# Performance work log

Measured on AMD Instinct MI355X. Metric: run time of the kernel, lower is better.

Reference implementation:

```python
import jax, jax.numpy as jnp
import numpy as np

EPS = 1e-8


def setup_inputs() -> dict:
    B, L, K = 512, 4096, 4
    key = jax.random.key(0)
    k1, k2, k3, k4 = jax.random.split(key, 4)
    # observations: Bernoulli-like values in [0,1] (math is valid for soft obs too)
    obs = (jax.random.uniform(k1, (B, L), dtype=jnp.float32) > 0.5).astype(jnp.float32)
    mask = jnp.ones((B, L), dtype=bool)
    # normalized HMM parameters, as _normalize_params produces
    start = jax.random.uniform(k2, (K,), dtype=jnp.float32) + EPS
    start = start / start.sum()
    trans = jax.random.uniform(k3, (K, K), dtype=jnp.float32) + EPS
    trans = trans / trans.sum(axis=1, keepdims=True)
    emission = jnp.clip(jax.random.uniform(k4, (K,), dtype=jnp.float32), EPS, 1.0 - EPS)
    return {"obs": obs, "mask": mask, "start": start, "trans": trans, "emission": emission}


def _forward_backward(obs, mask, start, trans, emission):
    B, L = obs.shape
    K = start.shape[0]
    # log Bernoulli emission: (B, L, K); masked (missing) positions contribute 0
    logp = jnp.log(emission + EPS)
    log1mp = jnp.log1p(-emission + EPS)
    logB = obs[:, :, None] * logp + (1.0 - obs[:, :, None]) * log1mp
    logB = jnp.where(mask[:, :, None], logB, 0.0)

    logA = jnp.log(trans + EPS)            # (K, K)
    logstart = jnp.log(start + EPS)        # (K,)

    logB_t = jnp.transpose(logB, (1, 0, 2))  # (L, B, K)

    # forward recurrence: alpha_t[j] = logsumexp_i(alpha_{t-1}[i] + logA[i,j]) + logB_t[j]
    alpha0 = logstart[None, :] + logB_t[0]  # (B, K)

    def fstep(alpha_prev, logb_t):
        a = jax.nn.logsumexp(alpha_prev[:, :, None] + logA[None, :, :], axis=1) + logb_t
        return a, a

    _, alphas = jax.lax.scan(fstep, alpha0, logB_t[1:])
    alpha = jnp.concatenate([alpha0[None], alphas], axis=0)  # (L, B, K)

    # backward recurrence: beta_t[i] = logsumexp_j(logA[i,j] + logB_{t+1}[j] + beta_{t+1}[j])
    betaL = jnp.zeros((B, K), dtype=obs.dtype)

    def bstep(beta_next, logb_next):
        b = jax.nn.logsumexp(logA[None, :, :] + (logb_next + beta_next)[:, None, :], axis=2)
        return b, b

    _, betas = jax.lax.scan(bstep, betaL, logB_t[1:], reverse=True)
    beta = jnp.concatenate([betas, betaL[None]], axis=0)  # (L, B, K)

    alpha = jnp.transpose(alpha, (1, 0, 2))  # (B, L, K)
    beta = jnp.transpose(beta, (1, 0, 2))    # (B, L, K)

    # per-sequence log-likelihood at last valid timestep
    lengths = mask.sum(axis=1).astype(jnp.int32)
    last_idx = jnp.clip(lengths - 1, 0, L - 1)
    final_alpha = alpha[jnp.arange(B), last_idx]  # (B, K)
    seq_loglikes = jax.nn.logsumexp(final_alpha, axis=1)

    # posterior marginals gamma = softmax(alpha + beta) over states
    gamma = jax.nn.softmax(alpha + beta, axis=-1)
    return gamma, seq_loglikes


def reference(obs, mask, start, trans, emission):
    return _forward_backward(obs, mask, start, trans, emission)
```

## Files before the change

kernel.cpp:

```cpp
#include <hip/hip_runtime.h>


#define BB 512
#define LL 4096
#define NT 512
#define SS 8
#define NW 8
#define EPSF 1e-8f
#define LN2F 0.6931471805599453f
#define HST 20

static_assert(NT * SS == LL, "chunking");

typedef float f4raw __attribute__((ext_vector_type(4)));

__device__ __forceinline__ float rcp_(float x) { return __builtin_amdgcn_rcpf(x); }
__device__ __forceinline__ float log_(float x) { return LN2F * __builtin_amdgcn_logf(x); }

__device__ __forceinline__ void mm16(const float* X, const float* Y, float* Z) {
#pragma unroll
    for (int i = 0; i < 4; i++)
#pragma unroll
        for (int j = 0; j < 4; j++)
            Z[i * 4 + j] = (X[i * 4 + 0] * Y[0 + j] + X[i * 4 + 1] * Y[4 + j]) +
                           (X[i * 4 + 2] * Y[8 + j] + X[i * 4 + 3] * Y[12 + j]);
}
__device__ __forceinline__ void nrm16(float* Z) {
    float s = 0.f;
#pragma unroll
    for (int k = 0; k < 16; k++) s += Z[k];
    float r = rcp_(s);
#pragma unroll
    for (int k = 0; k < 16; k++) Z[k] *= r;
}

__global__ __launch_bounds__(NT, 4) void k_fb(const float* __restrict__ obs,
                                              const float* __restrict__ start_,
                                              const float* __restrict__ trans,
                                              const float* __restrict__ emission,
                                              float* __restrict__ gamma,
                                              float* __restrict__ ll) {
    const int b = blockIdx.x;
    const int c = threadIdx.x;
    const int lane = c & 63;
    const int wv = c >> 6;

    __shared__ f4raw gbuf[NT * SS];
    __shared__ float H4[16][HST];
    __shared__ float H4f[16][HST];
    __shared__ float totF[NW][16];
    __shared__ float totB[NW][16];
    __shared__ float bndA[NW][4];
    __shared__ float bndB[NW][4];
    __shared__ float llred[NW];

    float A[16], pe[4], qe[4], sv[4];
#pragma unroll
    for (int k = 0; k < 16; k++) A[k] = trans[k] + EPSF;
#pragma unroll
    for (int j = 0; j < 4; j++) {
        float e = emission[j];
        pe[j] = e + EPSF;
        qe[j] = 1.0f - e + EPSF;
    }
    {
        float s = 0.f;
#pragma unroll
        for (int j = 0; j < 4; j++) { sv[j] = start_[j] + EPSF; s += sv[j]; }
        float r = rcp_(s);
#pragma unroll
        for (int j = 0; j < 4; j++) sv[j] *= r;
    }

    const float4* op = (const float4*)(obs + (size_t)b * LL + c * SS);
    float4 oa = op[0], ob2 = op[1];
    unsigned bits = (oa.x > 0.5f ? 1u : 0u) | (oa.y > 0.5f ? 2u : 0u) |
                    (oa.z > 0.5f ? 4u : 0u) | (oa.w > 0.5f ? 8u : 0u) |
                    (ob2.x > 0.5f ? 16u : 0u) | (ob2.y > 0.5f ? 32u : 0u) |
                    (ob2.z > 0.5f ? 64u : 0u) | (ob2.w > 0.5f ? 128u : 0u);

    if (c < 32) {
        const int o = c & 15;
        const bool first = c >= 16;
        float Mt[16];
        {
            float b0[4];
            int o0 = o & 1;
#pragma unroll
            for (int j = 0; j < 4; j++) b0[j] = o0 ? pe[j] : qe[j];
            if (first) {
#pragma unroll
                for (int k = 0; k < 16; k++) Mt[k] = 0.f;
#pragma unroll
                for (int j = 0; j < 4; j++) Mt[j * 4 + j] = b0[j];
            } else {
#pragma unroll
                for (int i = 0; i < 4; i++)
#pragma unroll
                    for (int j = 0; j < 4; j++) Mt[i * 4 + j] = A[i * 4 + j] * b0[j];
            }
        }
#pragma unroll
        for (int u = 1; u < 4; u++) {
            int ou = (o >> u) & 1;
            float bu[4];
#pragma unroll
            for (int j = 0; j < 4; j++) bu[j] = ou ? pe[j] : qe[j];
            float Zt[16];
#pragma unroll
            for (int i = 0; i < 4; i++)
#pragma unroll
                for (int j = 0; j < 4; j++)
                    Zt[i * 4 + j] = ((Mt[i * 4 + 0] * A[0 + j] + Mt[i * 4 + 1] * A[4 + j]) +
                                     (Mt[i * 4 + 2] * A[8 + j] + Mt[i * 4 + 3] * A[12 + j])) * bu[j];
#pragma unroll
            for (int k = 0; k < 16; k++) Mt[k] = Zt[k];
        }
        nrm16(Mt);
        float* dst = first ? &H4f[o][0] : &H4[o][0];
#pragma unroll
        for (int k = 0; k < 16; k++) dst[k] = Mt[k];
    }
    __syncthreads();

    float P[16];
    {
        const int i1 = bits & 15, i2 = (bits >> 4) & 15;
        const float* Xp = (c == 0) ? &H4f[i1][0] : &H4[i1][0];
        float X[16], Y[16];
#pragma unroll
        for (int k = 0; k < 16; k++) { X[k] = Xp[k]; Y[k] = H4[i2][k]; }
        mm16(X, Y, P);
        nrm16(P);
    }

    float M[16];
#pragma unroll
    for (int k = 0; k < 16; k++) M[k] = P[k];
#pragma unroll
    for (int d = 1; d < 64; d <<= 1) {
        int src = lane - d;
        int s2 = src < 0 ? 0 : src;
        float Up[16];
#pragma unroll
        for (int r = 0; r < 16; r++) Up[r] = __shfl(M[r], s2, 64);
        float Z[16];
        mm16(Up, M, Z);
        bool ok = lane >= d;
#pragma unroll
        for (int k = 0; k < 16; k++) M[k] = ok ? Z[k] : M[k];
        if (d == 2 || d == 8 || d == 32) nrm16(M);
    }
    if (lane == 63) {
#pragma unroll
        for (int r = 0; r < 16; r++) totF[wv][r] = M[r];
    }
    __syncthreads();
    if (wv > 0) {
        float E[16];
#pragma unroll
        for (int k = 0; k < 16; k++) E[k] = totF[0][k];
        for (int w = 1; w < wv; w++) {
            float Z[16];
            mm16(E, &totF[w][0], Z);
#pragma unroll
            for (int k = 0; k < 16; k++) E[k] = Z[k];
        }
        float Z[16];
        mm16(E, M, Z);
#pragma unroll
        for (int k = 0; k < 16; k++) M[k] = Z[k];
    }
    nrm16(M);
    float vprev[4];
    {
        float vn[4];
#pragma unroll
        for (int j = 0; j < 4; j++)
            vn[j] = (sv[0] * M[0 + j] + sv[1] * M[4 + j]) +
                    (sv[2] * M[8 + j] + sv[3] * M[12 + j]);
        float r = rcp_((vn[0] + vn[1]) + (vn[2] + vn[3]));
#pragma unroll
        for (int j = 0; j < 4; j++) vn[j] *= r;
#pragma unroll
        for (int j = 0; j < 4; j++) vprev[j] = __shfl_up(vn[j], 1, 64);
        if (lane == 63) {
#pragma unroll
            for (int j = 0; j < 4; j++) bndA[wv][j] = vn[j];
        }
    }

#pragma unroll
    for (int k = 0; k < 16; k++) M[k] = P[k];
#pragma unroll
    for (int d = 1; d < 64; d <<= 1) {
        int src = lane + d;
        int s2 = src > 63 ? 63 : src;
        float Rt[16];
#pragma unroll
        for (int r = 0; r < 16; r++) Rt[r] = __shfl(M[r], s2, 64);
        float Z[16];
        mm16(M, Rt, Z);
        bool ok = (lane + d) <= 63;
#pragma unroll
        for (int k = 0; k < 16; k++) M[k] = ok ? Z[k] : M[k];
        if (d == 2 || d == 8 || d == 32) nrm16(M);
    }
    if (lane == 0) {
#pragma unroll
        for (int r = 0; r < 16; r++) totB[wv][r] = M[r];
    }
    __syncthreads();
    if (wv < NW - 1) {
        float S[16];
#pragma unroll
        for (int k = 0; k < 16; k++) S[k] = totB[wv + 1][k];
        for (int w = wv + 2; w < NW; w++) {
            float Z[16];
            mm16(S, &totB[w][0], Z);
#pragma unroll
            for (int k = 0; k < 16; k++) S[k] = Z[k];
        }
        float Z[16];
        mm16(M, S, Z);
#pragma unroll
        for (int k = 0; k < 16; k++) M[k] = Z[k];
    }
    nrm16(M);
    float bnext[4];
    {
        float un[4];
#pragma unroll
        for (int i = 0; i < 4; i++)
            un[i] = (M[i * 4 + 0] + M[i * 4 + 1]) + (M[i * 4 + 2] + M[i * 4 + 3]);
        float r = rcp_((un[0] + un[1]) + (un[2] + un[3]));
#pragma unroll
        for (int i = 0; i < 4; i++) un[i] *= r;
#pragma unroll
        for (int i = 0; i < 4; i++) bnext[i] = __shfl_down(un[i], 1, 64);
        if (lane == 0) {
#pragma unroll
            for (int i = 0; i < 4; i++) bndB[wv][i] = un[i];
        }
    }
    __syncthreads();

    float av[4];
#pragma unroll
    for (int j = 0; j < 4; j++) av[j] = vprev[j];
    if (lane == 0 && wv > 0) {
#pragma unroll
        for (int j = 0; j < 4; j++) av[j] = bndA[wv - 1][j];
    }
    if (c == 0) {
#pragma unroll
        for (int j = 0; j < 4; j++) av[j] = sv[j];
    }
    float be[4];
#pragma unroll
    for (int i = 0; i < 4; i++) be[i] = bnext[i];
    if (lane == 63 && wv < NW - 1) {
#pragma unroll
        for (int i = 0; i < 4; i++) be[i] = bndB[wv + 1][i];
    }
    if (c == NT - 1) {
#pragma unroll
        for (int i = 0; i < 4; i++) be[i] = 1.0f;
    }

    const int lrow = wv * 512 + lane * SS;
    float llp = 0.f;
#pragma unroll
    for (int s = 0; s < SS; s++) {
        float bb[4];
#pragma unroll
        for (int j = 0; j < 4; j++) bb[j] = ((bits >> s) & 1u) ? pe[j] : qe[j];
        float w[4];
        if (s == 0 && c == 0) {
#pragma unroll
            for (int j = 0; j < 4; j++) w[j] = av[j] * bb[j];
        } else {
#pragma unroll
            for (int j = 0; j < 4; j++)
                w[j] = ((av[0] * A[0 + j] + av[1] * A[4 + j]) +
                        (av[2] * A[8 + j] + av[3] * A[12 + j])) * bb[j];
        }
#pragma unroll
        for (int j = 0; j < 4; j++) av[j] = w[j];
        f4raw st; st.x = av[0]; st.y = av[1]; st.z = av[2]; st.w = av[3];
        gbuf[lrow + (s ^ (lane & 7))] = st;
        if (s == 3 || s == SS - 1) {
            float sm = (av[0] + av[1]) + (av[2] + av[3]);
            llp += log_(sm);
            float r = rcp_(sm);
#pragma unroll
            for (int j = 0; j < 4; j++) av[j] *= r;
        }
    }

#pragma unroll
    for (int s = SS - 1; s >= 0; s--) {
        const int idx = lrow + (s ^ (lane & 7));
        f4raw avv = gbuf[idx];
        float g0 = avv.x * be[0], g1 = avv.y * be[1];
        float g2 = avv.z * be[2], g3 = avv.w * be[3];
        float rg = rcp_((g0 + g1) + (g2 + g3));
        f4raw gv; gv.x = g0 * rg; gv.y = g1 * rg; gv.z = g2 * rg; gv.w = g3 * rg;
        gbuf[idx] = gv;

        float bb[4];
#pragma unroll
        for (int j = 0; j < 4; j++) bb[j] = ((bits >> s) & 1u) ? pe[j] : qe[j];
        float e0 = bb[0] * be[0], e1 = bb[1] * be[1];
        float e2 = bb[2] * be[2], e3 = bb[3] * be[3];
#pragma unroll
        for (int i = 0; i < 4; i++)
            be[i] = (A[i * 4 + 0] * e0 + A[i * 4 + 1] * e1) +
                    (A[i * 4 + 2] * e2 + A[i * 4 + 3] * e3);
        if (s == 4 || s == 0) {
            float r = rcp_((be[0] + be[1]) + (be[2] + be[3]));
#pragma unroll
            for (int i = 0; i < 4; i++) be[i] *= r;
        }
    }

    {
        f4raw* gout = (f4raw*)gamma + (size_t)b * 4096 + wv * 512;
#pragma unroll
        for (int k = 0; k < SS; k++) {
            int i = k * 64 + lane;
            int owner = i >> 3;
            int sw = (i & 7) ^ (owner & 7);
            f4raw v = gbuf[wv * 512 + owner * 8 + sw];
            __builtin_nontemporal_store(v, gout + i);
        }
    }

#pragma unroll
    for (int off = 32; off > 0; off >>= 1) llp += __shfl_down(llp, off, 64);
    if (lane == 0) llred[wv] = llp;
    __syncthreads();
    if (c == 0) {
        float t = 0.f;
#pragma unroll
        for (int w = 0; w < NW; w++) t += llred[w];
        ll[b] = t;
    }
}

extern "C" void kernel_launch(void* const* d_in, const int* in_sizes, int n_in,
                              void* d_out, int out_size, void* d_ws, size_t ws_size,
                              hipStream_t stream) {
    const float* obs      = (const float*)d_in[0];
    const float* start    = (const float*)d_in[2];
    const float* trans    = (const float*)d_in[3];
    const float* emission = (const float*)d_in[4];

    float* out   = (float*)d_out;
    float* gamma = out;
    float* ll    = out + (size_t)BB * LL * 4;

    k_fb<<<dim3(BB), dim3(NT), 0, stream>>>(obs, start, trans, emission, gamma, ll);
}
```

Baseline: 98.14 us.

## Split fused forward-backward kernel into scan and replay kernels via workspace

Splits the single kernel into two. A scan kernel computes per-chunk forward and backward boundary vectors and writes them to workspace memory. It also computes the log-likelihood from tracked log-scale factors rather than a per-step reduction. A replay kernel then runs with 256-thread blocks and twice as many blocks, recomputes the local recurrences and writes gamma. This is meant to shrink the LDS footprint and register pressure so more blocks fit per CU, at the cost of a second launch, re-reading obs and a workspace round trip.

```diff
diff --git a/kernel.cpp b/kernel.cpp
--- a/kernel.cpp
+++ b/kernel.cpp
@@ -3,14 +3,15 @@
 
 #define BB 512
 #define LL 4096
-#define NT 512
+#define NT1 512
 #define SS 8
-#define NW 8
+#define NW1 8
+#define NT2 256
 #define EPSF 1e-8f
 #define LN2F 0.6931471805599453f
 #define HST 20
 
-static_assert(NT * SS == LL, "chunking");
+static_assert(NT1 * SS == LL, "chunking");
 
 typedef float f4raw __attribute__((ext_vector_type(4)));
 
@@ -25,44 +26,37 @@
             Z[i * 4 + j] = (X[i * 4 + 0] * Y[0 + j] + X[i * 4 + 1] * Y[4 + j]) +
                            (X[i * 4 + 2] * Y[8 + j] + X[i * 4 + 3] * Y[12 + j]);
 }
-__device__ __forceinline__ void nrm16(float* Z) {
+__device__ __forceinline__ float nrm16s(float* Z) {
     float s = 0.f;
 #pragma unroll
     for (int k = 0; k < 16; k++) s += Z[k];
     float r = rcp_(s);
 #pragma unroll
     for (int k = 0; k < 16; k++) Z[k] *= r;
-}
-
-__global__ __launch_bounds__(NT, 4) void k_fb(const float* __restrict__ obs,
-                                              const float* __restrict__ start_,
-                                              const float* __restrict__ trans,
-                                              const float* __restrict__ emission,
-                                              float* __restrict__ gamma,
-                                              float* __restrict__ ll) {
+    return s;
+}
+
+__global__ __launch_bounds__(NT1, 4) void k_scan(const float* __restrict__ obs,
+                                                 const float* __restrict__ start_,
+                                                 const float* __restrict__ trans,
+                                                 const float* __restrict__ emission,
+                                                 f4raw* __restrict__ a_in,
+                                                 f4raw* __restrict__ b_in,
+                                                 float* __restrict__ ll) {
     const int b = blockIdx.x;
     const int c = threadIdx.x;
     const int lane = c & 63;
     const int wv = c >> 6;
 
-    __shared__ f4raw gbuf[NT * SS];
     __shared__ float H4[16][HST];
     __shared__ float H4f[16][HST];
-    __shared__ float totF[NW][16];
-    __shared__ float totB[NW][16];
-    __shared__ float bndA[NW][4];
-    __shared__ float bndB[NW][4];
-    __shared__ float llred[NW];
-
-    float A[16], pe[4], qe[4], sv[4];
-#pragma unroll
-    for (int k = 0; k < 16; k++) A[k] = trans[k] + EPSF;
-#pragma unroll
-    for (int j = 0; j < 4; j++) {
-        float e = emission[j];
-        pe[j] = e + EPSF;
-        qe[j] = 1.0f - e + EPSF;
-    }
+    __shared__ float totF[NW1][17];
+    __shared__ float totB[NW1][16];
+
+    const float4* op = (const float4*)(obs + (size_t)b * LL + c * SS);
+    float4 oa = op[0], ob2 = op[1];
+
+    float sv[4];
     {
         float s = 0.f;
 #pragma unroll
@@ -72,14 +66,21 @@
         for (int j = 0; j < 4; j++) sv[j] *= r;
     }
 
-    const float4* op = (const float4*)(obs + (size_t)b * LL + c * SS);
-    float4 oa = op[0], ob2 = op[1];
     unsigned bits = (oa.x > 0.5f ? 1u : 0u) | (oa.y > 0.5f ? 2u : 0u) |
                     (oa.z > 0.5f ? 4u : 0u) | (oa.w > 0.5f ? 8u : 0u) |
                     (ob2.x > 0.5f ? 16u : 0u) | (ob2.y > 0.5f ? 32u : 0u) |
                     (ob2.z > 0.5f ? 64u : 0u) | (ob2.w > 0.5f ? 128u : 0u);
 
     if (c < 32) {
+        float A[16], pe[4], qe[4];
+#pragma unroll
+        for (int k = 0; k < 16; k++) A[k] = trans[k] + EPSF;
+#pragma unroll
+        for (int j = 0; j < 4; j++) {
+            float e = emission[j];
+            pe[j] = e + EPSF;
+            qe[j] = 1.0f - e + EPSF;
+        }
         const int o = c & 15;
         const bool first = c >= 16;
         float Mt[16];
@@ -116,25 +117,25 @@
 #pragma unroll
             for (int k = 0; k < 16; k++) Mt[k] = Zt[k];
         }
-        nrm16(Mt);
+        float s = nrm16s(Mt);
         float* dst = first ? &H4f[o][0] : &H4[o][0];
 #pragma unroll
         for (int k = 0; k < 16; k++) dst[k] = Mt[k];
+        dst[16] = log_(s);
     }
     __syncthreads();
 
     float P[16];
+    float Lp;
     {
         const int i1 = bits & 15, i2 = (bits >> 4) & 15;
         const float* Xp = (c == 0) ? &H4f[i1][0] : &H4[i1][0];
-        float X[16], Y[16];
-#pragma unroll
-        for (int k = 0; k < 16; k++) { X[k] = Xp[k]; Y[k] = H4[i2][k]; }
-        mm16(X, Y, P);
-        nrm16(P);
-    }
-
-    float M[16];
+        const float* Yp = &H4[i2][0];
+        mm16(Xp, Yp, P);
+        Lp = Xp[16] + Yp[16] + log_(nrm16s(P));
+    }
+
+    float M[16], Lm = Lp;
 #pragma unroll
     for (int k = 0; k < 16; k++) M[k] = P[k];
 #pragma unroll
@@ -144,25 +145,30 @@
         float Up[16];
 #pragma unroll
         for (int r = 0; r < 16; r++) Up[r] = __shfl(M[r], s2, 64);
+        float Lup = __shfl(Lm, s2, 64);
         float Z[16];
         mm16(Up, M, Z);
         bool ok = lane >= d;
 #pragma unroll
         for (int k = 0; k < 16; k++) M[k] = ok ? Z[k] : M[k];
-        if (d == 2 || d == 8 || d == 32) nrm16(M);
+        Lm = ok ? (Lup + Lm) : Lm;
+        if (d == 2 || d == 8 || d == 32) Lm += log_(nrm16s(M));
     }
     if (lane == 63) {
 #pragma unroll
         for (int r = 0; r < 16; r++) totF[wv][r] = M[r];
+        totF[wv][16] = Lm;
     }
     __syncthreads();
     if (wv > 0) {
         float E[16];
+        float LE = totF[0][16];
 #pragma unroll
         for (int k = 0; k < 16; k++) E[k] = totF[0][k];
         for (int w = 1; w < wv; w++) {
             float Z[16];
             mm16(E, &totF[w][0], Z);
+            LE += totF[w][16];
 #pragma unroll
             for (int k = 0; k < 16; k++) E[k] = Z[k];
         }
@@ -170,23 +176,28 @@
         mm16(E, M, Z);
 #pragma unroll
         for (int k = 0; k < 16; k++) M[k] = Z[k];
-    }
-    nrm16(M);
-    float vprev[4];
+        Lm += LE;
+    }
+    Lm += log_(nrm16s(M));
+
     {
         float vn[4];
 #pragma unroll
         for (int j = 0; j < 4; j++)
             vn[j] = (sv[0] * M[0 + j] + sv[1] * M[4 + j]) +
                     (sv[2] * M[8 + j] + sv[3] * M[12 + j]);
-        float r = rcp_((vn[0] + vn[1]) + (vn[2] + vn[3]));
-#pragma unroll
-        for (int j = 0; j < 4; j++) vn[j] *= r;
-#pragma unroll
-        for (int j = 0; j < 4; j++) vprev[j] = __shfl_up(vn[j], 1, 64);
-        if (lane == 63) {
-#pragma unroll
-            for (int j = 0; j < 4; j++) bndA[wv][j] = vn[j];
+        float s = (vn[0] + vn[1]) + (vn[2] + vn[3]);
+        f4raw* arow = a_in + (size_t)b * NT1;
+        if (c == NT1 - 1) {
+            ll[b] = log_(s) + Lm;
+        } else {
+            float r = rcp_(s);
+            f4raw v; v.x = vn[0] * r; v.y = vn[1] * r; v.z = vn[2] * r; v.w = vn[3] * r;
+            arow[c + 1] = v;
+        }
+        if (c == 0) {
+            f4raw v; v.x = sv[0]; v.y = sv[1]; v.z = sv[2]; v.w = sv[3];
+            arow[0] = v;
         }
     }
 
@@ -204,18 +215,18 @@
         bool ok = (lane + d) <= 63;
 #pragma unroll
         for (int k = 0; k < 16; k++) M[k] = ok ? Z[k] : M[k];
-        if (d == 2 || d == 8 || d == 32) nrm16(M);
+        if (d == 2 || d == 8 || d == 32) nrm16s(M);
     }
     if (lane == 0) {
 #pragma unroll
         for (int r = 0; r < 16; r++) totB[wv][r] = M[r];
     }
     __syncthreads();
-    if (wv < NW - 1) {
+    if (wv < NW1 - 1) {
         float S[16];
 #pragma unroll
         for (int k = 0; k < 16; k++) S[k] = totB[wv + 1][k];
-        for (int w = wv + 2; w < NW; w++) {
+        for (int w = wv + 2; w < NW1; w++) {
             float Z[16];
             mm16(S, &totB[w][0], Z);
 #pragma unroll
@@ -226,50 +237,63 @@
 #pragma unroll
         for (int k = 0; k < 16; k++) M[k] = Z[k];
     }
-    nrm16(M);
-    float bnext[4];
+    nrm16s(M);
     {
         float un[4];
 #pragma unroll
         for (int i = 0; i < 4; i++)
             un[i] = (M[i * 4 + 0] + M[i * 4 + 1]) + (M[i * 4 + 2] + M[i * 4 + 3]);
         float r = rcp_((un[0] + un[1]) + (un[2] + un[3]));
-#pragma unroll
-        for (int i = 0; i < 4; i++) un[i] *= r;
-#pragma unroll
-        for (int i = 0; i < 4; i++) bnext[i] = __shfl_down(un[i], 1, 64);
-        if (lane == 0) {
-#pragma unroll
-            for (int i = 0; i < 4; i++) bndB[wv][i] = un[i];
-        }
-    }
-    __syncthreads();
-
-    float av[4];
-#pragma unroll
-    for (int j = 0; j < 4; j++) av[j] = vprev[j];
-    if (lane == 0 && wv > 0) {
-#pragma unroll
-        for (int j = 0; j < 4; j++) av[j] = bndA[wv - 1][j];
-    }
-    if (c == 0) {
-#pragma unroll
-        for (int j = 0; j < 4; j++) av[j] = sv[j];
-    }
-    float be[4];
-#pragma unroll
-    for (int i = 0; i < 4; i++) be[i] = bnext[i];
-    if (lane == 63 && wv < NW - 1) {
-#pragma unroll
-        for (int i = 0; i < 4; i++) be[i] = bndB[wv + 1][i];
-    }
-    if (c == NT - 1) {
-#pragma unroll
-        for (int i = 0; i < 4; i++) be[i] = 1.0f;
-    }
+        f4raw* brow = b_in + (size_t)b * NT1;
+        if (c > 0) {
+            f4raw v; v.x = un[0] * r; v.y = un[1] * r; v.z = un[2] * r; v.w = un[3] * r;
+            brow[c - 1] = v;
+        }
+        if (c == NT1 - 1) {
+            f4raw v; v.x = 1.f; v.y = 1.f; v.z = 1.f; v.w = 1.f;
+            brow[NT1 - 1] = v;
+        }
+    }
+}
+
+__global__ __launch_bounds__(NT2, 4) void k_replay(const float* __restrict__ obs,
+                                                   const float* __restrict__ trans,
+                                                   const float* __restrict__ emission,
+                                                   const f4raw* __restrict__ a_in,
+                                                   const f4raw* __restrict__ b_in,
+                                                   float* __restrict__ gamma) {
+    const int bid = blockIdx.x;
+    const int b = bid >> 1;
+    const int h = bid & 1;
+    const int t = threadIdx.x;
+    const int lane = t & 63;
+    const int wv = t >> 6;
+    const int c = h * NT2 + t;
+
+    __shared__ f4raw gbuf[NT2 * SS];
+
+    float A[16], pe[4], qe[4];
+#pragma unroll
+    for (int k = 0; k < 16; k++) A[k] = trans[k] + EPSF;
+#pragma unroll
+    for (int j = 0; j < 4; j++) {
+        float e = emission[j];
+        pe[j] = e + EPSF;
+        qe[j] = 1.0f - e + EPSF;
+    }
+
+    const float4* op = (const float4*)(obs + (size_t)b * LL + (size_t)c * SS);
+    float4 oa = op[0], ob2 = op[1];
+    unsigned bits = (oa.x > 0.5f ? 1u : 0u) | (oa.y > 0.5f ? 2u : 0u) |
+                    (oa.z > 0.5f ? 4u : 0u) | (oa.w > 0.5f ? 8u : 0u) |
+                    (ob2.x > 0.5f ? 16u : 0u) | (ob2.y > 0.5f ? 32u : 0u) |
+                    (ob2.z > 0.5f ? 64u : 0u) | (ob2.w > 0.5f ? 128u : 0u);
+
+    f4raw av4 = a_in[(size_t)b * NT1 + c];
+    f4raw be4 = b_in[(size_t)b * NT1 + c];
+    float av[4] = {av4.x, av4.y, av4.z, av4.w};
 
     const int lrow = wv * 512 + lane * SS;
-    float llp = 0.f;
 #pragma unroll
     for (int s = 0; s < SS; s++) {
         float bb[4];
@@ -289,15 +313,14 @@
         for (int j = 0; j < 4; j++) av[j] = w[j];
         f4raw st; st.x = av[0]; st.y = av[1]; st.z = av[2]; st.w = av[3];
         gbuf[lrow + (s ^ (lane & 7))] = st;
-        if (s == 3 || s == SS - 1) {
-            float sm = (av[0] + av[1]) + (av[2] + av[3]);
-            llp += log_(sm);
-            float r = rcp_(sm);
+        if ((s & 3) == 3) {
+            float r = rcp_((av[0] + av[1]) + (av[2] + av[3]));
 #pragma unroll
             for (int j = 0; j < 4; j++) av[j] *= r;
         }
     }
 
+    float be[4] = {be4.x, be4.y, be4.z, be4.w};
 #pragma unroll
     for (int s = SS - 1; s >= 0; s--) {
         const int idx = lrow + (s ^ (lane & 7));
@@ -317,7 +340,7 @@
         for (int i = 0; i < 4; i++)
             be[i] = (A[i * 4 + 0] * e0 + A[i * 4 + 1] * e1) +
                     (A[i * 4 + 2] * e2 + A[i * 4 + 3] * e3);
-        if (s == 4 || s == 0) {
+        if ((s & 3) == 0) {
             float r = rcp_((be[0] + be[1]) + (be[2] + be[3]));
 #pragma unroll
             for (int i = 0; i < 4; i++) be[i] *= r;
@@ -325,7 +348,7 @@
     }
 
     {
-        f4raw* gout = (f4raw*)gamma + (size_t)b * 4096 + wv * 512;
+        f4raw* gout = (f4raw*)gamma + (size_t)b * 4096 + h * 2048 + wv * 512;
 #pragma unroll
         for (int k = 0; k < SS; k++) {
             int i = k * 64 + lane;
@@ -334,17 +357,6 @@
             f4raw v = gbuf[wv * 512 + owner * 8 + sw];
             __builtin_nontemporal_store(v, gout + i);
         }
-    }
-
-#pragma unroll
-    for (int off = 32; off > 0; off >>= 1) llp += __shfl_down(llp, off, 64);
-    if (lane == 0) llred[wv] = llp;
-    __syncthreads();
-    if (c == 0) {
-        float t = 0.f;
-#pragma unroll
-        for (int w = 0; w < NW; w++) t += llred[w];
-        ll[b] = t;
     }
 }
 
@@ -360,5 +372,9 @@
     float* gamma = out;
     float* ll    = out + (size_t)BB * LL * 4;
 
-    k_fb<<<dim3(BB), dim3(NT), 0, stream>>>(obs, start, trans, emission, gamma, ll);
-}
+    f4raw* a_in = (f4raw*)d_ws;
+    f4raw* b_in = a_in + (size_t)BB * NT1;
+
+    k_scan<<<dim3(BB), dim3(NT1), 0, stream>>>(obs, start, trans, emission, a_in, b_in, ll);
+    k_replay<<<dim3(2 * BB), dim3(NT2), 0, stream>>>(obs, trans, emission, a_in, b_in, gamma);
+}
```

After: 107.3 us. 9.4% more time.

## Build chunk matrices directly per thread and fuse forward/backward wave scans

Applied to the files above, without the earlier changes.

Each thread now computes its 8-step transfer matrix directly instead of going through a shared table of 4-step lookup matrices, which removes one block barrier and the shared-memory lookup. The forward and backward 64-lane shuffle scans are interleaved in a single loop, and the two separate barrier phases are merged into one. The log-likelihood is carried as an accumulated log-scale through the scan, so the final shuffle and shared reduction plus their barrier go away. The cost is more per-thread FLOPs for the matrix build and higher register pressure from holding both scan matrices at once.

```diff
diff --git a/kernel.cpp b/kernel.cpp
--- a/kernel.cpp
+++ b/kernel.cpp
@@ -8,7 +8,6 @@
 #define NW 8
 #define EPSF 1e-8f
 #define LN2F 0.6931471805599453f
-#define HST 20
 
 static_assert(NT * SS == LL, "chunking");
 
@@ -25,13 +24,14 @@
             Z[i * 4 + j] = (X[i * 4 + 0] * Y[0 + j] + X[i * 4 + 1] * Y[4 + j]) +
                            (X[i * 4 + 2] * Y[8 + j] + X[i * 4 + 3] * Y[12 + j]);
 }
-__device__ __forceinline__ void nrm16(float* Z) {
+__device__ __forceinline__ float nrm16s(float* Z) {
     float s = 0.f;
 #pragma unroll
     for (int k = 0; k < 16; k++) s += Z[k];
     float r = rcp_(s);
 #pragma unroll
     for (int k = 0; k < 16; k++) Z[k] *= r;
+    return s;
 }
 
 __global__ __launch_bounds__(NT, 4) void k_fb(const float* __restrict__ obs,
@@ -46,15 +46,203 @@
     const int wv = c >> 6;
 
     __shared__ f4raw gbuf[NT * SS];
-    __shared__ float H4[16][HST];
-    __shared__ float H4f[16][HST];
-    __shared__ float totF[NW][16];
+    __shared__ float totF[NW][17];
     __shared__ float totB[NW][16];
-    __shared__ float bndA[NW][4];
-    __shared__ float bndB[NW][4];
-    __shared__ float llred[NW];
-
-    float A[16], pe[4], qe[4], sv[4];
+
+    const float4* op = (const float4*)(obs + (size_t)b * LL + c * SS);
+    float4 oa = op[0], ob2 = op[1];
+
+    float sv[4];
+    {
+        float s = 0.f;
+#pragma unroll
+        for (int j = 0; j < 4; j++) { sv[j] = start_[j] + EPSF; s += sv[j]; }
+        float r = rcp_(s);
+#pragma unroll
+        for (int j = 0; j < 4; j++) sv[j] *= r;
+    }
+
+    unsigned bits = (oa.x > 0.5f ? 1u : 0u) | (oa.y > 0.5f ? 2u : 0u) |
+                    (oa.z > 0.5f ? 4u : 0u) | (oa.w > 0.5f ? 8u : 0u) |
+                    (ob2.x > 0.5f ? 16u : 0u) | (ob2.y > 0.5f ? 32u : 0u) |
+                    (ob2.z > 0.5f ? 64u : 0u) | (ob2.w > 0.5f ? 128u : 0u);
+
+    float P[16];
+    float Lp = 0.f;
+    {
+        float A[16], pe[4], qe[4];
+#pragma unroll
+        for (int k = 0; k < 16; k++) A[k] = trans[k] + EPSF;
+#pragma unroll
+        for (int j = 0; j < 4; j++) {
+            float e = emission[j];
+            pe[j] = e + EPSF;
+            qe[j] = 1.0f - e + EPSF;
+        }
+        {
+            float bb[4];
+#pragma unroll
+            for (int j = 0; j < 4; j++) bb[j] = (bits & 1u) ? pe[j] : qe[j];
+            if (c == 0) {
+#pragma unroll
+                for (int i = 0; i < 4; i++)
+#pragma unroll
+                    for (int j = 0; j < 4; j++) P[i * 4 + j] = (i == j) ? bb[j] : 0.f;
+            } else {
+#pragma unroll
+                for (int i = 0; i < 4; i++)
+#pragma unroll
+                    for (int j = 0; j < 4; j++) P[i * 4 + j] = A[i * 4 + j] * bb[j];
+            }
+        }
+#pragma unroll
+        for (int s = 1; s < SS; s++) {
+            float bb[4];
+#pragma unroll
+            for (int j = 0; j < 4; j++) bb[j] = ((bits >> s) & 1u) ? pe[j] : qe[j];
+            float T[16];
+#pragma unroll
+            for (int i = 0; i < 4; i++)
+#pragma unroll
+                for (int j = 0; j < 4; j++)
+                    T[i * 4 + j] = ((P[i * 4 + 0] * A[0 + j] + P[i * 4 + 1] * A[4 + j]) +
+                                    (P[i * 4 + 2] * A[8 + j] + P[i * 4 + 3] * A[12 + j])) * bb[j];
+#pragma unroll
+            for (int k = 0; k < 16; k++) P[k] = T[k];
+            if (s == 3 || s == SS - 1) Lp += log_(nrm16s(P));
+        }
+    }
+
+    float Mf[16], Mb[16], Lm = Lp;
+#pragma unroll
+    for (int k = 0; k < 16; k++) { Mf[k] = P[k]; Mb[k] = P[k]; }
+#pragma unroll
+    for (int d = 1; d < 64; d <<= 1) {
+        const int sF = (lane >= d) ? (lane - d) : 0;
+        const int sB = (lane + d <= 63) ? (lane + d) : 63;
+        float UF[16], UB[16];
+#pragma unroll
+        for (int r = 0; r < 16; r++) UF[r] = __shfl(Mf[r], sF, 64);
+        float LF = __shfl(Lm, sF, 64);
+#pragma unroll
+        for (int r = 0; r < 16; r++) UB[r] = __shfl(Mb[r], sB, 64);
+        float Z[16];
+        mm16(UF, Mf, Z);
+        const bool okF = (lane >= d);
+#pragma unroll
+        for (int k = 0; k < 16; k++) Mf[k] = okF ? Z[k] : Mf[k];
+        Lm = okF ? (LF + Lm) : Lm;
+        mm16(Mb, UB, Z);
+        const bool okB = (lane + d <= 63);
+#pragma unroll
+        for (int k = 0; k < 16; k++) Mb[k] = okB ? Z[k] : Mb[k];
+        if (d == 2 || d == 8 || d == 32) { Lm += log_(nrm16s(Mf)); nrm16s(Mb); }
+    }
+    if (lane == 63) {
+#pragma unroll
+        for (int r = 0; r < 16; r++) totF[wv][r] = Mf[r];
+        totF[wv][16] = Lm;
+    }
+    if (lane == 0) {
+#pragma unroll
+        for (int r = 0; r < 16; r++) totB[wv][r] = Mb[r];
+    }
+    __syncthreads();
+
+    float vprev[4];
+    {
+        float E[16];
+        if (wv > 0) {
+            float LE = totF[0][16];
+#pragma unroll
+            for (int k = 0; k < 16; k++) E[k] = totF[0][k];
+            for (int w = 1; w < wv; w++) {
+                float Z[16];
+                mm16(E, &totF[w][0], Z);
+                LE += totF[w][16];
+#pragma unroll
+                for (int k = 0; k < 16; k++) E[k] = Z[k];
+            }
+            float Z[16];
+            mm16(E, Mf, Z);
+#pragma unroll
+            for (int k = 0; k < 16; k++) Mf[k] = Z[k];
+            Lm += LE;
+        }
+        Lm += log_(nrm16s(Mf));
+        float vn[4];
+#pragma unroll
+        for (int j = 0; j < 4; j++)
+            vn[j] = (sv[0] * Mf[0 + j] + sv[1] * Mf[4 + j]) +
+                    (sv[2] * Mf[8 + j] + sv[3] * Mf[12 + j]);
+        float s = (vn[0] + vn[1]) + (vn[2] + vn[3]);
+        if (c == NT - 1) ll[b] = log_(s) + Lm;
+        float r = rcp_(s);
+#pragma unroll
+        for (int j = 0; j < 4; j++) vn[j] *= r;
+#pragma unroll
+        for (int j = 0; j < 4; j++) vprev[j] = __shfl_up(vn[j], 1, 64);
+        if (lane == 0) {
+            if (wv == 0) {
+#pragma unroll
+                for (int j = 0; j < 4; j++) vprev[j] = sv[j];
+            } else {
+                float vp[4];
+#pragma unroll
+                for (int j = 0; j < 4; j++)
+                    vp[j] = (sv[0] * E[0 + j] + sv[1] * E[4 + j]) +
+                            (sv[2] * E[8 + j] + sv[3] * E[12 + j]);
+                float rr = rcp_((vp[0] + vp[1]) + (vp[2] + vp[3]));
+#pragma unroll
+                for (int j = 0; j < 4; j++) vprev[j] = vp[j] * rr;
+            }
+        }
+    }
+
+    float bnext[4];
+    {
+        float S[16];
+        if (wv < NW - 1) {
+#pragma unroll
+            for (int k = 0; k < 16; k++) S[k] = totB[wv + 1][k];
+            for (int w = wv + 2; w < NW; w++) {
+                float Z[16];
+                mm16(S, &totB[w][0], Z);
+#pragma unroll
+                for (int k = 0; k < 16; k++) S[k] = Z[k];
+            }
+            float Z[16];
+            mm16(Mb, S, Z);
+#pragma unroll
+            for (int k = 0; k < 16; k++) Mb[k] = Z[k];
+        }
+        nrm16s(Mb);
+        float u[4];
+#pragma unroll
+        for (int i = 0; i < 4; i++)
+            u[i] = (Mb[i * 4 + 0] + Mb[i * 4 + 1]) + (Mb[i * 4 + 2] + Mb[i * 4 + 3]);
+        float r = rcp_((u[0] + u[1]) + (u[2] + u[3]));
+#pragma unroll
+        for (int i = 0; i < 4; i++) u[i] *= r;
+#pragma unroll
+        for (int i = 0; i < 4; i++) bnext[i] = __shfl_down(u[i], 1, 64);
+        if (lane == 63) {
+            if (wv == NW - 1) {
+#pragma unroll
+                for (int i = 0; i < 4; i++) bnext[i] = 0.25f;
+            } else {
+                float bn[4];
+#pragma unroll
+                for (int i = 0; i < 4; i++)
+                    bn[i] = (S[i * 4 + 0] + S[i * 4 + 1]) + (S[i * 4 + 2] + S[i * 4 + 3]);
+                float rr = rcp_((bn[0] + bn[1]) + (bn[2] + bn[3]));
+#pragma unroll
+                for (int i = 0; i < 4; i++) bnext[i] = bn[i] * rr;
+            }
+        }
+    }
+
+    float A[16], pe[4], qe[4];
 #pragma unroll
     for (int k = 0; k < 16; k++) A[k] = trans[k] + EPSF;
 #pragma unroll
@@ -63,213 +251,11 @@
         pe[j] = e + EPSF;
         qe[j] = 1.0f - e + EPSF;
     }
-    {
-        float s = 0.f;
-#pragma unroll
-        for (int j = 0; j < 4; j++) { sv[j] = start_[j] + EPSF; s += sv[j]; }
-        float r = rcp_(s);
-#pragma unroll
-        for (int j = 0; j < 4; j++) sv[j] *= r;
-    }
-
-    const float4* op = (const float4*)(obs + (size_t)b * LL + c * SS);
-    float4 oa = op[0], ob2 = op[1];
-    unsigned bits = (oa.x > 0.5f ? 1u : 0u) | (oa.y > 0.5f ? 2u : 0u) |
-                    (oa.z > 0.5f ? 4u : 0u) | (oa.w > 0.5f ? 8u : 0u) |
-                    (ob2.x > 0.5f ? 16u : 0u) | (ob2.y > 0.5f ? 32u : 0u) |
-                    (ob2.z > 0.5f ? 64u : 0u) | (ob2.w > 0.5f ? 128u : 0u);
-
-    if (c < 32) {
-        const int o = c & 15;
-        const bool first = c >= 16;
-        float Mt[16];
-        {
-            float b0[4];
-            int o0 = o & 1;
-#pragma unroll
-            for (int j = 0; j < 4; j++) b0[j] = o0 ? pe[j] : qe[j];
-            if (first) {
-#pragma unroll
-                for (int k = 0; k < 16; k++) Mt[k] = 0.f;
-#pragma unroll
-                for (int j = 0; j < 4; j++) Mt[j * 4 + j] = b0[j];
-            } else {
-#pragma unroll
-                for (int i = 0; i < 4; i++)
-#pragma unroll
-                    for (int j = 0; j < 4; j++) Mt[i * 4 + j] = A[i * 4 + j] * b0[j];
-            }
-        }
-#pragma unroll
-        for (int u = 1; u < 4; u++) {
-            int ou = (o >> u) & 1;
-            float bu[4];
-#pragma unroll
-            for (int j = 0; j < 4; j++) bu[j] = ou ? pe[j] : qe[j];
-            float Zt[16];
-#pragma unroll
-            for (int i = 0; i < 4; i++)
-#pragma unroll
-                for (int j = 0; j < 4; j++)
-                    Zt[i * 4 + j] = ((Mt[i * 4 + 0] * A[0 + j] + Mt[i * 4 + 1] * A[4 + j]) +
-                                     (Mt[i * 4 + 2] * A[8 + j] + Mt[i * 4 + 3] * A[12 + j])) * bu[j];
-#pragma unroll
-            for (int k = 0; k < 16; k++) Mt[k] = Zt[k];
-        }
-        nrm16(Mt);
-        float* dst = first ? &H4f[o][0] : &H4[o][0];
-#pragma unroll
-        for (int k = 0; k < 16; k++) dst[k] = Mt[k];
-    }
-    __syncthreads();
-
-    float P[16];
-    {
-        const int i1 = bits & 15, i2 = (bits >> 4) & 15;
-        const float* Xp = (c == 0) ? &H4f[i1][0] : &H4[i1][0];
-        float X[16], Y[16];
-#pragma unroll
-        for (int k = 0; k < 16; k++) { X[k] = Xp[k]; Y[k] = H4[i2][k]; }
-        mm16(X, Y, P);
-        nrm16(P);
-    }
-
-    float M[16];
-#pragma unroll
-    for (int k = 0; k < 16; k++) M[k] = P[k];
-#pragma unroll
-    for (int d = 1; d < 64; d <<= 1) {
-        int src = lane - d;
-        int s2 = src < 0 ? 0 : src;
-        float Up[16];
-#pragma unroll
-        for (int r = 0; r < 16; r++) Up[r] = __shfl(M[r], s2, 64);
-        float Z[16];
-        mm16(Up, M, Z);
-        bool ok = lane >= d;
-#pragma unroll
-        for (int k = 0; k < 16; k++) M[k] = ok ? Z[k] : M[k];
-        if (d == 2 || d == 8 || d == 32) nrm16(M);
-    }
-    if (lane == 63) {
-#pragma unroll
-        for (int r = 0; r < 16; r++) totF[wv][r] = M[r];
-    }
-    __syncthreads();
-    if (wv > 0) {
-        float E[16];
-#pragma unroll
-        for (int k = 0; k < 16; k++) E[k] = totF[0][k];
-        for (int w = 1; w < wv; w++) {
-            float Z[16];
-            mm16(E, &totF[w][0], Z);
-#pragma unroll
-            for (int k = 0; k < 16; k++) E[k] = Z[k];
-        }
-        float Z[16];
-        mm16(E, M, Z);
-#pragma unroll
-        for (int k = 0; k < 16; k++) M[k] = Z[k];
-    }
-    nrm16(M);
-    float vprev[4];
-    {
-        float vn[4];
-#pragma unroll
-        for (int j = 0; j < 4; j++)
-            vn[j] = (sv[0] * M[0 + j] + sv[1] * M[4 + j]) +
-                    (sv[2] * M[8 + j] + sv[3] * M[12 + j]);
-        float r = rcp_((vn[0] + vn[1]) + (vn[2] + vn[3]));
-#pragma unroll
-        for (int j = 0; j < 4; j++) vn[j] *= r;
-#pragma unroll
-        for (int j = 0; j < 4; j++) vprev[j] = __shfl_up(vn[j], 1, 64);
-        if (lane == 63) {
-#pragma unroll
-            for (int j = 0; j < 4; j++) bndA[wv][j] = vn[j];
-        }
-    }
-
-#pragma unroll
-    for (int k = 0; k < 16; k++) M[k] = P[k];
-#pragma unroll
-    for (int d = 1; d < 64; d <<= 1) {
-        int src = lane + d;
-        int s2 = src > 63 ? 63 : src;
-        float Rt[16];
-#pragma unroll
-        for (int r = 0; r < 16; r++) Rt[r] = __shfl(M[r], s2, 64);
-        float Z[16];
-        mm16(M, Rt, Z);
-        bool ok = (lane + d) <= 63;
-#pragma unroll
-        for (int k = 0; k < 16; k++) M[k] = ok ? Z[k] : M[k];
-        if (d == 2 || d == 8 || d == 32) nrm16(M);
-    }
-    if (lane == 0) {
-#pragma unroll
-        for (int r = 0; r < 16; r++) totB[wv][r] = M[r];
-    }
-    __syncthreads();
-    if (wv < NW - 1) {
-        float S[16];
-#pragma unroll
-        for (int k = 0; k < 16; k++) S[k] = totB[wv + 1][k];
-        for (int w = wv + 2; w < NW; w++) {
-            float Z[16];
-            mm16(S, &totB[w][0], Z);
-#pragma unroll
-            for (int k = 0; k < 16; k++) S[k] = Z[k];
-        }
-        float Z[16];
-        mm16(M, S, Z);
-#pragma unroll
-        for (int k = 0; k < 16; k++) M[k] = Z[k];
-    }
-    nrm16(M);
-    float bnext[4];
-    {
-        float un[4];
-#pragma unroll
-        for (int i = 0; i < 4; i++)
-            un[i] = (M[i * 4 + 0] + M[i * 4 + 1]) + (M[i * 4 + 2] + M[i * 4 + 3]);
-        float r = rcp_((un[0] + un[1]) + (un[2] + un[3]));
-#pragma unroll
-        for (int i = 0; i < 4; i++) un[i] *= r;
-#pragma unroll
-        for (int i = 0; i < 4; i++) bnext[i] = __shfl_down(un[i], 1, 64);
-        if (lane == 0) {
-#pragma unroll
-            for (int i = 0; i < 4; i++) bndB[wv][i] = un[i];
-        }
-    }
-    __syncthreads();
 
     float av[4];
 #pragma unroll
     for (int j = 0; j < 4; j++) av[j] = vprev[j];
-    if (lane == 0 && wv > 0) {
-#pragma unroll
-        for (int j = 0; j < 4; j++) av[j] = bndA[wv - 1][j];
-    }
-    if (c == 0) {
-#pragma unroll
-        for (int j = 0; j < 4; j++) av[j] = sv[j];
-    }
-    float be[4];
-#pragma unroll
-    for (int i = 0; i < 4; i++) be[i] = bnext[i];
-    if (lane == 63 && wv < NW - 1) {
-#pragma unroll
-        for (int i = 0; i < 4; i++) be[i] = bndB[wv + 1][i];
-    }
-    if (c == NT - 1) {
-#pragma unroll
-        for (int i = 0; i < 4; i++) be[i] = 1.0f;
-    }
-
     const int lrow = wv * 512 + lane * SS;
-    float llp = 0.f;
 #pragma unroll
     for (int s = 0; s < SS; s++) {
         float bb[4];
@@ -289,15 +275,16 @@
         for (int j = 0; j < 4; j++) av[j] = w[j];
         f4raw st; st.x = av[0]; st.y = av[1]; st.z = av[2]; st.w = av[3];
         gbuf[lrow + (s ^ (lane & 7))] = st;
-        if (s == 3 || s == SS - 1) {
-            float sm = (av[0] + av[1]) + (av[2] + av[3]);
-            llp += log_(sm);
-            float r = rcp_(sm);
+        if ((s & 3) == 3) {
+            float r = rcp_((av[0] + av[1]) + (av[2] + av[3]));
 #pragma unroll
             for (int j = 0; j < 4; j++) av[j] *= r;
         }
     }
 
+    float be[4];
+#pragma unroll
+    for (int i = 0; i < 4; i++) be[i] = bnext[i];
 #pragma unroll
     for (int s = SS - 1; s >= 0; s--) {
         const int idx = lrow + (s ^ (lane & 7));
@@ -317,7 +304,7 @@
         for (int i = 0; i < 4; i++)
             be[i] = (A[i * 4 + 0] * e0 + A[i * 4 + 1] * e1) +
                     (A[i * 4 + 2] * e2 + A[i * 4 + 3] * e3);
-        if (s == 4 || s == 0) {
+        if ((s & 3) == 0) {
             float r = rcp_((be[0] + be[1]) + (be[2] + be[3]));
 #pragma unroll
             for (int i = 0; i < 4; i++) be[i] *= r;
@@ -334,17 +321,6 @@
             f4raw v = gbuf[wv * 512 + owner * 8 + sw];
             __builtin_nontemporal_store(v, gout + i);
         }
-    }
-
-#pragma unroll
-    for (int off = 32; off > 0; off >>= 1) llp += __shfl_down(llp, off, 64);
-    if (lane == 0) llred[wv] = llp;
-    __syncthreads();
-    if (c == 0) {
-        float t = 0.f;
-#pragma unroll
-        for (int w = 0; w < NW; w++) t += llred[w];
-        ll[b] = t;
     }
 }
 
```

Measured after the change: 98.55 us. About the same (+0.4%).
